# Optimization experiments

Hardware: AMD Instinct MI355X
Metric: run time of the kernel (lower is better)

## Reference

```python
import jax, jax.numpy as jnp
import numpy as np

B, S, D, H = 2, 2048, 2048, 16
HD = D // H          # head_dim = 128
FF = 8192            # intermediate_size
LN_EPS = 1e-05
BIT_EPS = 1e-05


def _rope_tables(seq_len, head_dim):
    inv_freq = 1.0 / (10000.0 ** (np.arange(0, head_dim, 2, dtype=np.float64) / head_dim))
    ang = np.arange(seq_len, dtype=np.float64)[:, None] * inv_freq[None, :]  # [S, HD/2]
    ang = np.concatenate([ang, ang], axis=-1)  # [S, HD]
    return jnp.asarray(np.cos(ang), jnp.float32), jnp.asarray(np.sin(ang), jnp.float32)


def setup_inputs() -> dict:
    key = jax.random.key(0)
    ks = jax.random.split(key, 9)
    hidden_states = jax.random.normal(ks[0], (B, S, D), jnp.float32)
    # causal additive mask [1, S, S]
    causal = jnp.tril(jnp.ones((S, S), bool))
    attention_mask = jnp.where(causal, 0.0, -1e9)[None].astype(jnp.float32)
    cos, sin = _rope_tables(S, HD)
    w = lambda k, o, i: jax.random.normal(k, (o, i), jnp.float32) * 0.02
    return {
        'hidden_states': hidden_states,
        'attention_mask': attention_mask,
        'cos': cos, 'sin': sin,
        'wq': w(ks[1], D, D), 'wk': w(ks[2], D, D),
        'wv': w(ks[3], D, D), 'wo': w(ks[4], D, D),
        'wg': w(ks[5], FF, D), 'wu': w(ks[6], FF, D), 'wd': w(ks[7], D, FF),
        'ln1_w': jnp.ones((D,), jnp.float32),
        'ln2_w': jnp.ones((D,), jnp.float32),
    }


def bitlinear(x, w):
    # ternarize: clamp(round(w / (mean|w| + eps)), -1, 1); int8 cast in torch
    # breaks grad through the ternary values -> stop_gradient here.
    scale = jnp.mean(jnp.abs(w))
    tern = jax.lax.stop_gradient(jnp.clip(jnp.round(w / (scale + BIT_EPS)), -1.0, 1.0))
    # dequant = ternary * mean|w|, then standard linear (x @ W^T)
    return jnp.einsum('bsi,oi->bso', x, tern * scale)


def rmsnorm(x, w, eps=LN_EPS):
    var = jnp.mean(jnp.square(x.astype(jnp.float32)), axis=-1, keepdims=True)
    return w * (x * jax.lax.rsqrt(var + eps))


def rotate_half(x):
    x1, x2 = jnp.split(x, 2, axis=-1)
    return jnp.concatenate([-x2, x1], axis=-1)


def apply_rope(q, k, cos, sin):
    # q, k: [B, S, D] -> per-head rope -> back to [B, S, D]
    qh = q.reshape(B, S, H, HD)
    kh = k.reshape(B, S, H, HD)
    c = cos[None, :, None, :]
    s = sin[None, :, None, :]
    qe = qh * c + rotate_half(qh) * s
    ke = kh * c + rotate_half(kh) * s
    return qe.reshape(B, S, D), ke.reshape(B, S, D)


def reference(hidden_states, attention_mask, cos, sin,
              wq, wk, wv, wo, wg, wu, wd, ln1_w, ln2_w):
    residual = hidden_states
    # --- attention block ---
    x = rmsnorm(hidden_states, ln1_w)
    q = bitlinear(x, wq)
    k = bitlinear(x, wk)
    v = bitlinear(x, wv)
    q, k = apply_rope(q, k, cos, sin)
    # NOTE: scores over FULL hidden dim (no head split), scaled by sqrt(head_dim),
    # exactly as in the original module.
    scores = jnp.einsum('bsd,btd->bst', q, k) / jnp.sqrt(jnp.float32(HD))
    scores = scores + attention_mask
    probs = jax.nn.softmax(scores, axis=-1)
    attn_out = jnp.einsum('bst,btd->bsd', probs, v)
    attn_out = bitlinear(attn_out, wo)
    h = residual + attn_out
    # --- MLP block ---
    residual = h
    y = rmsnorm(h, ln2_w)
    gated = bitlinear(y, wg) * bitlinear(y, wu)
    out = bitlinear(gated, wd)
    return residual + out
```

## Files before the change

### kernel.cpp

```cpp
#include <hip/hip_runtime.h>
#include <stdint.h>

#define DEV __device__ __forceinline__

typedef __attribute__((ext_vector_type(8))) short short8;
typedef __attribute__((ext_vector_type(8))) __bf16 bf16x8;
typedef __attribute__((ext_vector_type(4))) float f32x4;

DEV unsigned short f2bf(float f) {
  union { float f; unsigned int u; } v; v.f = f;
  unsigned int r = v.u + 0x7fffu + ((v.u >> 16) & 1u);
  return (unsigned short)(r >> 16);
}
DEV float bf2f(unsigned short h) {
  union { unsigned int u; float f; } v; v.u = ((unsigned int)h) << 16;
  return v.f;
}
DEV f32x4 mfma16(short8 a, short8 b, f32x4 c) {
  return __builtin_amdgcn_mfma_f32_16x16x32_bf16(
      __builtin_bit_cast(bf16x8, a), __builtin_bit_cast(bf16x8, b), c, 0, 0, 0);
}
DEV void gload_lds16(const void* g, void* lds) {
  __builtin_amdgcn_global_load_lds(
      (const __attribute__((address_space(1))) void*)g,
      (__attribute__((address_space(3))) void*)lds, 16, 0, 0);
}

struct MArgs {
  const float* src[7];
  unsigned short* dst[7];
  int n[7];
  int sidx[7];
};

__global__ __launch_bounds__(256) void absmean_partial_multi(
    MArgs a, float* __restrict__ partial) {
  const int m = blockIdx.y;
  const float4* w4 = (const float4*)a.src[m];
  const int n4 = a.n[m] >> 2;
  float s = 0.f;
  for (int i = blockIdx.x * 256 + threadIdx.x; i < n4; i += 1024 * 256) {
    float4 v = w4[i];
    s += fabsf(v.x) + fabsf(v.y) + fabsf(v.z) + fabsf(v.w);
  }
#pragma unroll
  for (int mm = 1; mm < 64; mm <<= 1) s += __shfl_xor(s, mm);
  __shared__ float red[4];
  if ((threadIdx.x & 63) == 0) red[threadIdx.x >> 6] = s;
  __syncthreads();
  if (threadIdx.x == 0)
    partial[m * 1024 + blockIdx.x] = red[0] + red[1] + red[2] + red[3];
}

__global__ __launch_bounds__(256) void absmean_final(
    const float* __restrict__ partial, float* __restrict__ scales) {
  __shared__ double red[256];
  const int m = blockIdx.x;
  double s = 0.0;
  for (int i = threadIdx.x; i < 1024; i += 256) s += (double)partial[m * 1024 + i];
  red[threadIdx.x] = s;
  __syncthreads();
  for (int t = 128; t > 0; t >>= 1) {
    if (threadIdx.x < t) red[threadIdx.x] += red[threadIdx.x + t];
    __syncthreads();
  }
  if (threadIdx.x == 0) {
    const long long cnt = (m < 4) ? 4194304ll : 16777216ll;
    scales[m] = (float)(red[0] / (double)cnt);
  }
}

__global__ __launch_bounds__(256) void quantize_multi(
    MArgs a, const float* __restrict__ scales) {
  const int m = blockIdx.y;
  const float sc = scales[a.sidx[m]];
  const float inv = 1.f / (sc + 1e-5f);
  const float4* src = (const float4*)a.src[m];
  ushort4* dst = (ushort4*)a.dst[m];
  const int n4 = a.n[m] >> 2;
  for (int i = blockIdx.x * 256 + threadIdx.x; i < n4; i += 2048 * 256) {
    float4 v = src[i];
    ushort4 o;
    o.x = f2bf(fminf(fmaxf(rintf(v.x * inv), -1.f), 1.f) * sc);
    o.y = f2bf(fminf(fmaxf(rintf(v.y * inv), -1.f), 1.f) * sc);
    o.z = f2bf(fminf(fmaxf(rintf(v.z * inv), -1.f), 1.f) * sc);
    o.w = f2bf(fminf(fmaxf(rintf(v.w * inv), -1.f), 1.f) * sc);
    dst[i] = o;
  }
}

__global__ __launch_bounds__(256) void rmsnorm_k(
    const float* __restrict__ x, const float* __restrict__ wt,
    unsigned short* __restrict__ out) {
  const long long t = blockIdx.x;
  const float* xr = x + t * 2048;
  const int i0 = threadIdx.x * 8;
  float4 a = *(const float4*)(xr + i0);
  float4 b = *(const float4*)(xr + i0 + 4);
  float ss = a.x * a.x + a.y * a.y + a.z * a.z + a.w * a.w +
             b.x * b.x + b.y * b.y + b.z * b.z + b.w * b.w;
#pragma unroll
  for (int m = 1; m < 64; m <<= 1) ss += __shfl_xor(ss, m);
  __shared__ float red[4];
  if ((threadIdx.x & 63) == 0) red[threadIdx.x >> 6] = ss;
  __syncthreads();
  float tot = red[0] + red[1] + red[2] + red[3];
  float rs = rsqrtf(tot * (1.f / 2048.f) + 1e-5f);
  float4 wa = *(const float4*)(wt + i0);
  float4 wb = *(const float4*)(wt + i0 + 4);
  ushort4 o1, o2;
  o1.x = f2bf(a.x * wa.x * rs); o1.y = f2bf(a.y * wa.y * rs);
  o1.z = f2bf(a.z * wa.z * rs); o1.w = f2bf(a.w * wa.w * rs);
  o2.x = f2bf(b.x * wb.x * rs); o2.y = f2bf(b.y * wb.y * rs);
  o2.z = f2bf(b.z * wb.z * rs); o2.w = f2bf(b.w * wb.w * rs);
  *(ushort4*)(out + t * 2048 + i0) = o1;
  *(ushort4*)(out + t * 2048 + i0 + 4) = o2;
}

__global__ __launch_bounds__(256) void combine_rms(
    const float* __restrict__ ep, const unsigned short* __restrict__ p,
    const float* __restrict__ wt, float* __restrict__ hout,
    unsigned short* __restrict__ yout) {
  const long long t = blockIdx.x;
  const int i0 = threadIdx.x * 8;
  const long long base = t * 2048 + i0;
  float4 e1 = *(const float4*)(ep + base);
  float4 e2 = *(const float4*)(ep + base + 4);
  short8 pa = *(const short8*)(p + base);
  short8 pb = *(const short8*)(p + 8388608 + base);
  const float e[8] = {e1.x, e1.y, e1.z, e1.w, e2.x, e2.y, e2.z, e2.w};
  float h[8];
#pragma unroll
  for (int i = 0; i < 8; ++i)
    h[i] = e[i] + bf2f((unsigned short)pa[i]) + bf2f((unsigned short)pb[i]);
  float4 h1 = {h[0], h[1], h[2], h[3]};
  float4 h2 = {h[4], h[5], h[6], h[7]};
  *(float4*)(hout + base) = h1;
  *(float4*)(hout + base + 4) = h2;
  float ss = 0.f;
#pragma unroll
  for (int i = 0; i < 8; ++i) ss += h[i] * h[i];
#pragma unroll
  for (int m = 1; m < 64; m <<= 1) ss += __shfl_xor(ss, m);
  __shared__ float red[4];
  if ((threadIdx.x & 63) == 0) red[threadIdx.x >> 6] = ss;
  __syncthreads();
  const float tot = red[0] + red[1] + red[2] + red[3];
  const float rs = rsqrtf(tot * (1.f / 2048.f) + 1e-5f);
  float4 wa = *(const float4*)(wt + i0);
  float4 wb = *(const float4*)(wt + i0 + 4);
  ushort4 o1, o2;
  o1.x = f2bf(h[0] * wa.x * rs); o1.y = f2bf(h[1] * wa.y * rs);
  o1.z = f2bf(h[2] * wa.z * rs); o1.w = f2bf(h[3] * wa.w * rs);
  o2.x = f2bf(h[4] * wb.x * rs); o2.y = f2bf(h[5] * wb.y * rs);
  o2.z = f2bf(h[6] * wb.z * rs); o2.w = f2bf(h[7] * wb.w * rs);
  *(ushort4*)(yout + base) = o1;
  *(ushort4*)(yout + base + 4) = o2;
}

__global__ __launch_bounds__(256) void combine2(
    const float* __restrict__ ep, const unsigned short* __restrict__ p,
    float* __restrict__ out) {
  const long long base = (long long)blockIdx.x * 2048 + threadIdx.x * 8;
  float4 e1 = *(const float4*)(ep + base);
  float4 e2 = *(const float4*)(ep + base + 4);
  short8 pa = *(const short8*)(p + base);
  short8 pb = *(const short8*)(p + 8388608 + base);
  float4 o1, o2;
  o1.x = e1.x + bf2f((unsigned short)pa[0]) + bf2f((unsigned short)pb[0]);
  o1.y = e1.y + bf2f((unsigned short)pa[1]) + bf2f((unsigned short)pb[1]);
  o1.z = e1.z + bf2f((unsigned short)pa[2]) + bf2f((unsigned short)pb[2]);
  o1.w = e1.w + bf2f((unsigned short)pa[3]) + bf2f((unsigned short)pb[3]);
  o2.x = e2.x + bf2f((unsigned short)pa[4]) + bf2f((unsigned short)pb[4]);
  o2.y = e2.y + bf2f((unsigned short)pa[5]) + bf2f((unsigned short)pb[5]);
  o2.z = e2.z + bf2f((unsigned short)pa[6]) + bf2f((unsigned short)pb[6]);
  o2.w = e2.w + bf2f((unsigned short)pa[7]) + bf2f((unsigned short)pb[7]);
  *(float4*)(out + base) = o1;
  *(float4*)(out + base + 4) = o2;
}

__global__ __launch_bounds__(256) void rope_k(
    const unsigned short* __restrict__ qkv, const float* __restrict__ cosT,
    const float* __restrict__ sinT, unsigned short* __restrict__ qr,
    unsigned short* __restrict__ kr) {
  const long long gid = (long long)blockIdx.x * 256 + threadIdx.x;
  const int t = (int)(gid >> 10);
  const int r = (int)(gid & 1023);
  const int h = r >> 6, d = r & 63;
  const int s = t & 2047;
  const unsigned short* row = qkv + (long long)t * 6144;
  const float c = cosT[s * 128 + d], sn = sinT[s * 128 + d];
  const int col = h * 128 + d;
  const float SC = 0.08838834764831845f;
  float q1 = bf2f(row[col]), q2 = bf2f(row[col + 64]);
  float k1 = bf2f(row[2048 + col]), k2 = bf2f(row[2048 + col + 64]);
  long long ob = (long long)t * 2048 + col;
  qr[ob] = f2bf((q1 * c - q2 * sn) * SC);
  qr[ob + 64] = f2bf((q2 * c + q1 * sn) * SC);
  kr[ob] = f2bf(k1 * c - k2 * sn);
  kr[ob + 64] = f2bf(k2 * c + k1 * sn);
}

__global__ __launch_bounds__(256) void vtrans_k(
    const unsigned short* __restrict__ qkv, unsigned short* __restrict__ vt) {
  __shared__ unsigned short tile[64][66];
  const int tt = blockIdx.x << 6, dd = blockIdx.y << 6;
  const long long b = blockIdx.z;
  const int r0 = threadIdx.x >> 4, c0 = (threadIdx.x & 15) << 2;
#pragma unroll
  for (int i = 0; i < 4; ++i) {
    const int row = r0 + i * 16;
    ushort4 v = *(const ushort4*)&qkv[(b * 2048 + tt + row) * 6144 + 4096 + dd + c0];
    tile[row][c0] = v.x; tile[row][c0 + 1] = v.y;
    tile[row][c0 + 2] = v.z; tile[row][c0 + 3] = v.w;
  }
  __syncthreads();
#pragma unroll
  for (int i = 0; i < 4; ++i) {
    const int d = r0 + i * 16;
    ushort4 o;
    o.x = tile[c0][d]; o.y = tile[c0 + 1][d];
    o.z = tile[c0 + 2][d]; o.w = tile[c0 + 3][d];
    *(ushort4*)&vt[(b * 2048 + dd + d) * 2048 + tt + c0] = o;
  }
}

__global__ __launch_bounds__(256) void softmax_causal(
    const float* __restrict__ scores, unsigned short* __restrict__ probs) {
  const int r = blockIdx.x;
  const int s = r & 2047;
  const float* src = scores + (long long)r * 2048;
  unsigned short* dst = probs + (long long)r * 2048;
  const int L = s + 1;
  const int j0 = threadIdx.x * 8;
  float4 a = *(const float4*)(src + j0);
  float4 b = *(const float4*)(src + j0 + 4);
  float v[8] = {a.x, a.y, a.z, a.w, b.x, b.y, b.z, b.w};
  float mx = -1e30f;
#pragma unroll
  for (int i = 0; i < 8; ++i) {
    if (j0 + i >= L) v[i] = -1e30f;
    mx = fmaxf(mx, v[i]);
  }
#pragma unroll
  for (int m = 1; m < 64; m <<= 1) mx = fmaxf(mx, __shfl_xor(mx, m));
  __shared__ float redM[4], redS[4];
  if ((threadIdx.x & 63) == 0) redM[threadIdx.x >> 6] = mx;
  __syncthreads();
  mx = fmaxf(fmaxf(redM[0], redM[1]), fmaxf(redM[2], redM[3]));
  float sum = 0.f;
#pragma unroll
  for (int i = 0; i < 8; ++i) {
    v[i] = (j0 + i < L) ? __expf(v[i] - mx) : 0.f;
    sum += v[i];
  }
#pragma unroll
  for (int m = 1; m < 64; m <<= 1) sum += __shfl_xor(sum, m);
  if ((threadIdx.x & 63) == 0) redS[threadIdx.x >> 6] = sum;
  __syncthreads();
  const float inv = 1.f / (redS[0] + redS[1] + redS[2] + redS[3]);
  ushort4 o1, o2;
  o1.x = f2bf(v[0] * inv); o1.y = f2bf(v[1] * inv);
  o1.z = f2bf(v[2] * inv); o1.w = f2bf(v[3] * inv);
  o2.x = f2bf(v[4] * inv); o2.y = f2bf(v[5] * inv);
  o2.z = f2bf(v[6] * inv); o2.w = f2bf(v[7] * inv);
  *(ushort4*)(dst + j0) = o1;
  *(ushort4*)(dst + j0 + 4) = o2;
}

template <int EPI, int CAUSAL>
__global__ __launch_bounds__(256) void gemm_nt(
    const unsigned short* __restrict__ A, const unsigned short* __restrict__ Bw,
    void* __restrict__ Cp, int M, int N, int K,
    long long sAz, long long sBz, long long sCz) {
  const long long m0 = (long long)blockIdx.y * 128;
  const long long n0 = (long long)blockIdx.x * 128;
  if (CAUSAL == 1 && n0 > m0 + 127) return;
  __shared__ __align__(16) unsigned short sA[2][128 * 32];
  __shared__ __align__(16) unsigned short sB[2][128 * 32];
  const int tid = threadIdx.x;
  const int w = tid >> 6, l = tid & 63;
  const long long z = blockIdx.z;
  A += z * sAz;
  Bw += z * sBz;
  const long long cofs = z * sCz;
  const int wr = w >> 1, wc = w & 1;
  const int lrow = l & 15, lk = (l >> 4) * 8;

  f32x4 acc[4][4] = {};
  int nk = K >> 5;
  if (CAUSAL == 2) nk = (int)((m0 + 128) >> 5);
  int cur = 0;

  auto stage = [&](int buf, int k0) {
#pragma unroll
    for (int i = 0; i < 2; ++i) {
      const int flat = (w * 2 + i) * 64 + l;
      const int row = flat >> 2;
      const int col = (flat & 3) * 8;
      gload_lds16(&A[(m0 + row) * K + k0 + col], (char*)&sA[buf][0] + (w * 2 + i) * 1024);
      gload_lds16(&Bw[(n0 + row) * K + k0 + col], (char*)&sB[buf][0] + (w * 2 + i) * 1024);
    }
  };

  stage(0, 0);
  __syncthreads();
  for (int kt = 0; kt < nk; ++kt) {
    if (kt + 1 < nk) stage(cur ^ 1, (kt + 1) << 5);
    short8 af[4], bfr[4];
#pragma unroll
    for (int m = 0; m < 4; ++m)
      af[m] = *(const short8*)&sA[cur][(wr * 64 + m * 16 + lrow) * 32 + lk];
#pragma unroll
    for (int n = 0; n < 4; ++n)
      bfr[n] = *(const short8*)&sB[cur][(wc * 64 + n * 16 + lrow) * 32 + lk];
#pragma unroll
    for (int m = 0; m < 4; ++m)
#pragma unroll
      for (int n = 0; n < 4; ++n)
        acc[m][n] = mfma16(af[m], bfr[n], acc[m][n]);
    __syncthreads();
    cur ^= 1;
  }

  const int orow = (l >> 4) * 4, ocol = l & 15;
#pragma unroll
  for (int m = 0; m < 4; ++m)
#pragma unroll
    for (int n = 0; n < 4; ++n)
#pragma unroll
      for (int r = 0; r < 4; ++r) {
        long long gr = m0 + wr * 64 + m * 16 + orow + r;
        long long gc = n0 + wc * 64 + n * 16 + ocol;
        long long idx = cofs + gr * N + gc;
        float v = acc[m][n][r];
        if (EPI == 0) ((unsigned short*)Cp)[idx] = f2bf(v);
        else ((float*)Cp)[idx] = v;
      }
}

template <int EPI, int CAUSAL>
__global__ __launch_bounds__(512, 2) void gemm256(
    const unsigned short* __restrict__ A, const unsigned short* __restrict__ Bw,
    void* __restrict__ Cp, const void* __restrict__ Ep,
    int N, int K, int nbx, int kLen, int ngTot,
    long long sAz, long long sBz, long long zCout) {
  __shared__ __align__(16) unsigned short lds[4 * 2 * 8192];
  __shared__ __align__(16) unsigned short ldsDummy[512];
  const int tid = threadIdx.x;
  const int wid = tid >> 6, l = tid & 63;
  const int wr = wid >> 2, wcn = wid & 3;

  const int nwg = gridDim.x;
  const int q8 = nwg >> 3;
  const int lin = (blockIdx.x & 7) * q8 + (blockIdx.x >> 3);
  const int t32 = lin >> 5, r32 = lin & 31;
  const int tpr = nbx >> 3;
  const int tm = t32 / tpr, tn = t32 - tm * tpr;
  const long long m0 = (long long)(tm * 4 + (r32 >> 3)) * 256;
  const long long n0 = (long long)(tn * 8 + (r32 & 7)) * 256;
  if (CAUSAL == 1 && n0 > m0) return;
  const int z = blockIdx.z;
  A += z * sAz;
  Bw += z * sBz;
  const long long kbase = (long long)z * kLen;
  const long long zofs = (long long)z * zCout;
  int ng = ngTot;
  if (CAUSAL == 2) {
    const int lim = (int)((m0 + 256) >> 5);
    ng = lim < ng ? lim : ng;
  }

  const int stRow = (l >> 2);
  const int stCol = (((l & 3) ^ ((l >> 3) & 3))) * 8;
  auto stage = [&](int chunk, int sslot) {
    if (chunk < ng) {
      char* base = (char*)lds + (sslot * 2) * 16384;
      const long long kcol = kbase + (long long)chunk * 32 + stCol;
#pragma unroll
      for (int i = 0; i < 2; ++i) {
        const int row = (wid * 2 + i) * 16 + stRow;
        gload_lds16(&A[(m0 + row) * K + kcol], base + (wid * 2 + i) * 1024);
        gload_lds16(&Bw[(n0 + row) * K + kcol],
                    base + 16384 + (wid * 2 + i) * 1024);
      }
    } else {
#pragma unroll
      for (int i = 0; i < 4; ++i) gload_lds16(&A[m0 * K], (char*)ldsDummy);
    }
  };

  const int ar = l & 15;
  const int rj = ((l >> 4) ^ ((l >> 1) & 3)) << 4;
  const int aoff = (wr * 128 + ar) * 64 + rj;
  const int boff = (wcn * 64 + ar) * 64 + rj;

  f32x4 acc[8][4] = {};
  short8 aX[4], bX[4], aY[4], bY[4];

  stage(0, 0); stage(1, 1); stage(2, 2);
  asm volatile("s_waitcnt vmcnt(4)" ::: "memory");
  __builtin_amdgcn_s_barrier();
#pragma unroll
  for (int m = 0; m < 4; ++m)
    aX[m] = *(const short8*)((const char*)lds + aoff + m * 1024);
#pragma unroll
  for (int n = 0; n < 4; ++n)
    bX[n] = *(const short8*)((const char*)lds + 16384 + boff + n * 1024);

#define CHUNK_BODY(SLOT, NSLOT, SYNC, cur03, curB, nxt03, nxtB, cc)            \
  {                                                                            \
    const char* sAc = (const char*)lds + (SLOT * 2) * 16384;                   \
    const char* sAn = (const char*)lds + (NSLOT * 2) * 16384;                  \
    const char* sBn = (const char*)lds + (NSLOT * 2 + 1) * 16384;              \
    short8 a47[4];                                                             \
    _Pragma("unroll") for (int m = 0; m < 4; ++m)                              \
        a47[m] = *(const short8*)(sAc + aoff + 4096 + m * 1024);               \
    stage((cc) + 3, (SLOT + 3) & 3);                                           \
    __builtin_amdgcn_s_setprio(1);                                             \
    _Pragma("unroll") for (int m = 0; m < 4; ++m)                              \
      _Pragma("unroll") for (int n = 0; n < 4; ++n)                            \
          acc[m][n] = mfma16(cur03[m], curB[n], acc[m][n]);                    \
    __builtin_amdgcn_s_setprio(0);                                             \
    if (SYNC) {                                                                \
      asm volatile("s_waitcnt vmcnt(4)" ::: "memory");                         \
      __builtin_amdgcn_s_barrier();                                            \
    }                                                                          \
    _Pragma("unroll") for (int m = 0; m < 4; ++m)                              \
        nxt03[m] = *(const short8*)(sAn + aoff + m * 1024);                    \
    _Pragma("unroll") for (int n = 0; n < 4; ++n)                              \
        nxtB[n] = *(const short8*)(sBn + boff + n * 1024);                     \
    __builtin_amdgcn_s_setprio(1);                                             \
    _Pragma("unroll") for (int m = 0; m < 4; ++m)                              \
      _Pragma("unroll") for (int n = 0; n < 4; ++n)                            \
          acc[m + 4][n] = mfma16(a47[m], curB[n], acc[m + 4][n]);              \
    __builtin_amdgcn_s_setprio(0);                                             \
  }

  for (int c = 0; c < ng; c += 4) {
    CHUNK_BODY(0, 1, false, aX, bX, aY, bY, c);
    CHUNK_BODY(1, 2, true, aY, bY, aX, bX, c + 1);
    CHUNK_BODY(2, 3, false, aX, bX, aY, bY, c + 2);
    CHUNK_BODY(3, 0, true, aY, bY, aX, bX, c + 3);
  }
#undef CHUNK_BODY
  asm volatile("s_waitcnt vmcnt(0)" ::: "memory");
  __builtin_amdgcn_s_barrier();

  const int orow = (l >> 4) * 4, ocol = l & 15;
#pragma unroll
  for (int m = 0; m < 8; ++m)
#pragma unroll
    for (int n = 0; n < 4; ++n)
#pragma unroll
      for (int r = 0; r < 4; ++r) {
        const long long gr = m0 + wr * 128 + m * 16 + orow + r;
        const long long gc = n0 + wcn * 64 + n * 16 + ocol;
        const long long idx = zofs + gr * N + gc;
        const float v = acc[m][n][r];
        if (EPI == 0) {
          ((unsigned short*)Cp)[idx] = f2bf(v);
        } else if (EPI == 2) {
          ((unsigned short*)Cp)[idx] = f2bf(bf2f(((const unsigned short*)Ep)[idx]) * v);
        } else {
          ((float*)Cp)[idx] = v;
        }
      }
}

extern "C" void kernel_launch(void* const* d_in, const int* in_sizes, int n_in,
                              void* d_out, int out_size, void* d_ws, size_t ws_size,
                              hipStream_t stream) {
  (void)in_sizes; (void)n_in; (void)out_size; (void)ws_size;
  const float* hidden = (const float*)d_in[0];
  const float* cosT = (const float*)d_in[2];
  const float* sinT = (const float*)d_in[3];
  const float* wq = (const float*)d_in[4];
  const float* wk = (const float*)d_in[5];
  const float* wv = (const float*)d_in[6];
  const float* wo = (const float*)d_in[7];
  const float* wg = (const float*)d_in[8];
  const float* wu = (const float*)d_in[9];
  const float* wd = (const float*)d_in[10];
  const float* ln1 = (const float*)d_in[11];
  const float* ln2 = (const float*)d_in[12];

  const size_t MB = 1ull << 20;
  char* ws = (char*)d_ws;
  unsigned short* xn    = (unsigned short*)(ws + 0);
  unsigned short* wqkvq = (unsigned short*)(ws + 16 * MB);
  unsigned short* qkv   = (unsigned short*)(ws + 40 * MB);
  unsigned short* qrb   = (unsigned short*)(ws + 88 * MB);
  unsigned short* krb   = (unsigned short*)(ws + 104 * MB);
  unsigned short* vtb   = (unsigned short*)(ws + 120 * MB);
  float*          scoresB = (float*)(ws + 0);
  unsigned short* probsB  = (unsigned short*)(ws + 40 * MB);
  unsigned short* partb = (unsigned short*)(ws + 0);
  unsigned short* wgq   = (unsigned short*)(ws + 0);
  unsigned short* wuq   = (unsigned short*)(ws + 32 * MB);
  unsigned short* gbuf  = (unsigned short*)(ws + 64 * MB);
  unsigned short* attnb = (unsigned short*)(ws + 136 * MB);
  unsigned short* woq   = (unsigned short*)(ws + 152 * MB);
  float*          hbuf  = (float*)(ws + 160 * MB);
  unsigned short* ybuf  = (unsigned short*)(ws + 192 * MB);
  unsigned short* gated = (unsigned short*)(ws + 208 * MB);
  unsigned short* wdq   = (unsigned short*)(ws + 272 * MB);
  float* wspart         = (float*)(ws + 304 * MB);
  float* scales         = (float*)(ws + 304 * MB + 32768);

  MArgs am;
  am.src[0] = wq; am.src[1] = wk; am.src[2] = wv; am.src[3] = wo;
  am.src[4] = wg; am.src[5] = wu; am.src[6] = wd;
  am.n[0] = am.n[1] = am.n[2] = am.n[3] = 4194304;
  am.n[4] = am.n[5] = am.n[6] = 16777216;
  for (int i = 0; i < 7; ++i) { am.dst[i] = nullptr; am.sidx[i] = i; }
  absmean_partial_multi<<<dim3(1024, 7), 256, 0, stream>>>(am, wspart);
  absmean_final<<<7, 256, 0, stream>>>(wspart, scales);

  MArgs qe;
  qe.src[0] = wq; qe.dst[0] = wqkvq;            qe.n[0] = 4194304;  qe.sidx[0] = 0;
  qe.src[1] = wk; qe.dst[1] = wqkvq + 4194304;  qe.n[1] = 4194304;  qe.sidx[1] = 1;
  qe.src[2] = wv; qe.dst[2] = wqkvq + 8388608;  qe.n[2] = 4194304;  qe.sidx[2] = 2;
  qe.src[3] = wo; qe.dst[3] = woq;              qe.n[3] = 4194304;  qe.sidx[3] = 3;
  qe.src[4] = wd; qe.dst[4] = wdq;              qe.n[4] = 16777216; qe.sidx[4] = 6;
  qe.src[5] = wq; qe.dst[5] = nullptr; qe.n[5] = 0; qe.sidx[5] = 0;
  qe.src[6] = wq; qe.dst[6] = nullptr; qe.n[6] = 0; qe.sidx[6] = 0;
  quantize_multi<<<dim3(2048, 5), 256, 0, stream>>>(qe, scales);

  rmsnorm_k<<<4096, 256, 0, stream>>>(hidden, ln1, xn);

  gemm256<0, 0><<<dim3(384, 1, 1), 512, 0, stream>>>(
      xn, wqkvq, qkv, nullptr, 6144, 2048, 24, 2048, 64, 0, 0, 0);

  rope_k<<<16384, 256, 0, stream>>>(qkv, cosT, sinT, qrb, krb);
  vtrans_k<<<dim3(32, 32, 2), 256, 0, stream>>>(qkv, vtb);

  gemm_nt<4, 1><<<dim3(16, 16, 2), 256, 0, stream>>>(
      qrb, krb, scoresB, 2048, 2048, 2048, 4194304, 4194304, 4194304);
  softmax_causal<<<4096, 256, 0, stream>>>(scoresB, probsB);
  gemm_nt<0, 2><<<dim3(16, 16, 2), 256, 0, stream>>>(
      probsB, vtb, attnb, 2048, 2048, 2048, 4194304, 4194304, 4194304);

  gemm256<0, 0><<<dim3(128, 1, 2), 512, 0, stream>>>(
      attnb, woq, partb, nullptr, 2048, 2048, 8, 1024, 32, 0, 0, 8388608);
  combine_rms<<<4096, 256, 0, stream>>>(hidden, partb, ln2, hbuf, ybuf);

  MArgs ql;
  ql.src[0] = wg; ql.dst[0] = wgq; ql.n[0] = 16777216; ql.sidx[0] = 4;
  ql.src[1] = wu; ql.dst[1] = wuq; ql.n[1] = 16777216; ql.sidx[1] = 5;
  for (int i = 2; i < 7; ++i) { ql.src[i] = wg; ql.dst[i] = nullptr; ql.n[i] = 0; ql.sidx[i] = 0; }
  quantize_multi<<<dim3(2048, 2), 256, 0, stream>>>(ql, scales);

  gemm256<0, 0><<<dim3(512, 1, 1), 512, 0, stream>>>(
      ybuf, wgq, gbuf, nullptr, 8192, 2048, 32, 2048, 64, 0, 0, 0);
  gemm256<2, 0><<<dim3(512, 1, 1), 512, 0, stream>>>(
      ybuf, wuq, gated, gbuf, 8192, 2048, 32, 2048, 64, 0, 0, 0);

  gemm256<0, 0><<<dim3(128, 1, 2), 512, 0, stream>>>(
      gated, wdq, partb, nullptr, 2048, 8192, 8, 4096, 128, 0, 0, 8388608);
  combine2<<<4096, 256, 0, stream>>>(hbuf, partb, (float*)d_out);
}
```

Baseline: 772.5 us.

## Restructure gemm256 to double-buffered 64-wide K tiles with phased barriers

Replaces the 4-slot, 32-wide K-chunk pipeline in gemm256 with a 2-buffer scheme using 64-wide K tiles split into two halves. Each tile runs four MFMA phases separated by barriers, with LDS waits and priority bumps, while the next tile's halves are prefetched. The unused CAUSAL template path is dropped. The intent is a more regular schedule with larger K steps and fewer stalls, at the cost of more barriers per tile and shallower prefetch depth.

```diff
diff --git a/kernel.cpp b/kernel.cpp
--- a/kernel.cpp
+++ b/kernel.cpp
@@ -339,14 +339,13 @@
       }
 }
 
-template <int EPI, int CAUSAL>
+template <int EPI>
 __global__ __launch_bounds__(512, 2) void gemm256(
     const unsigned short* __restrict__ A, const unsigned short* __restrict__ Bw,
     void* __restrict__ Cp, const void* __restrict__ Ep,
-    int N, int K, int nbx, int kLen, int ngTot,
+    int N, int K, int nbx, int kLen, int NT,
     long long sAz, long long sBz, long long zCout) {
-  __shared__ __align__(16) unsigned short lds[4 * 2 * 8192];
-  __shared__ __align__(16) unsigned short ldsDummy[512];
+  __shared__ __align__(16) unsigned short lds[2 * 2 * 2 * 8192];
   const int tid = threadIdx.x;
   const int wid = tid >> 6, l = tid & 63;
   const int wr = wid >> 2, wcn = wid & 3;
@@ -359,93 +358,104 @@
   const int tm = t32 / tpr, tn = t32 - tm * tpr;
   const long long m0 = (long long)(tm * 4 + (r32 >> 3)) * 256;
   const long long n0 = (long long)(tn * 8 + (r32 & 7)) * 256;
-  if (CAUSAL == 1 && n0 > m0) return;
   const int z = blockIdx.z;
   A += z * sAz;
   Bw += z * sBz;
   const long long kbase = (long long)z * kLen;
   const long long zofs = (long long)z * zCout;
-  int ng = ngTot;
-  if (CAUSAL == 2) {
-    const int lim = (int)((m0 + 256) >> 5);
-    ng = lim < ng ? lim : ng;
-  }
-
-  const int stRow = (l >> 2);
-  const int stCol = (((l & 3) ^ ((l >> 3) & 3))) * 8;
-  auto stage = [&](int chunk, int sslot) {
-    if (chunk < ng) {
-      char* base = (char*)lds + (sslot * 2) * 16384;
-      const long long kcol = kbase + (long long)chunk * 32 + stCol;
-#pragma unroll
-      for (int i = 0; i < 2; ++i) {
-        const int row = (wid * 2 + i) * 16 + stRow;
-        gload_lds16(&A[(m0 + row) * K + kcol], base + (wid * 2 + i) * 1024);
-        gload_lds16(&Bw[(n0 + row) * K + kcol],
-                    base + 16384 + (wid * 2 + i) * 1024);
-      }
-    } else {
-#pragma unroll
-      for (int i = 0; i < 4; ++i) gload_lds16(&A[m0 * K], (char*)ldsDummy);
+
+  const int sRow = tid >> 2;
+  const int sCol = ((tid & 3) ^ ((sRow >> 1) & 3)) * 8;
+  auto stageH = [&](int tile, int matofs, int khalf, int bufofs) {
+    if (tile < NT) {
+      const unsigned short* src = matofs ? Bw : A;
+      const long long rb = matofs ? n0 : m0;
+      const long long kc = kbase + (long long)tile * 64 + khalf * 32 + sCol;
+      char* dst = (char*)lds + bufofs + matofs + khalf * 16384 + wid * 1024;
+      gload_lds16(&src[(rb + sRow) * K + kc], dst);
+      gload_lds16(&src[(rb + sRow + 128) * K + kc], dst + 8192);
     }
   };
 
   const int ar = l & 15;
   const int rj = ((l >> 4) ^ ((l >> 1) & 3)) << 4;
-  const int aoff = (wr * 128 + ar) * 64 + rj;
-  const int boff = (wcn * 64 + ar) * 64 + rj;
 
   f32x4 acc[8][4] = {};
-  short8 aX[4], bX[4], aY[4], bY[4];
-
-  stage(0, 0); stage(1, 1); stage(2, 2);
-  asm volatile("s_waitcnt vmcnt(4)" ::: "memory");
-  __builtin_amdgcn_s_barrier();
-#pragma unroll
-  for (int m = 0; m < 4; ++m)
-    aX[m] = *(const short8*)((const char*)lds + aoff + m * 1024);
-#pragma unroll
-  for (int n = 0; n < 4; ++n)
-    bX[n] = *(const short8*)((const char*)lds + 16384 + boff + n * 1024);
-
-#define CHUNK_BODY(SLOT, NSLOT, SYNC, cur03, curB, nxt03, nxtB, cc)            \
-  {                                                                            \
-    const char* sAc = (const char*)lds + (SLOT * 2) * 16384;                   \
-    const char* sAn = (const char*)lds + (NSLOT * 2) * 16384;                  \
-    const char* sBn = (const char*)lds + (NSLOT * 2 + 1) * 16384;              \
-    short8 a47[4];                                                             \
-    _Pragma("unroll") for (int m = 0; m < 4; ++m)                              \
-        a47[m] = *(const short8*)(sAc + aoff + 4096 + m * 1024);               \
-    stage((cc) + 3, (SLOT + 3) & 3);                                           \
-    __builtin_amdgcn_s_setprio(1);                                             \
-    _Pragma("unroll") for (int m = 0; m < 4; ++m)                              \
-      _Pragma("unroll") for (int n = 0; n < 4; ++n)                            \
-          acc[m][n] = mfma16(cur03[m], curB[n], acc[m][n]);                    \
-    __builtin_amdgcn_s_setprio(0);                                             \
-    if (SYNC) {                                                                \
-      asm volatile("s_waitcnt vmcnt(4)" ::: "memory");                         \
-      __builtin_amdgcn_s_barrier();                                            \
-    }                                                                          \
-    _Pragma("unroll") for (int m = 0; m < 4; ++m)                              \
-        nxt03[m] = *(const short8*)(sAn + aoff + m * 1024);                    \
-    _Pragma("unroll") for (int n = 0; n < 4; ++n)                              \
-        nxtB[n] = *(const short8*)(sBn + boff + n * 1024);                     \
-    __builtin_amdgcn_s_setprio(1);                                             \
-    _Pragma("unroll") for (int m = 0; m < 4; ++m)                              \
-      _Pragma("unroll") for (int n = 0; n < 4; ++n)                            \
-          acc[m + 4][n] = mfma16(a47[m], curB[n], acc[m + 4][n]);              \
-    __builtin_amdgcn_s_setprio(0);                                             \
-  }
-
-  for (int c = 0; c < ng; c += 4) {
-    CHUNK_BODY(0, 1, false, aX, bX, aY, bY, c);
-    CHUNK_BODY(1, 2, true, aY, bY, aX, bX, c + 1);
-    CHUNK_BODY(2, 3, false, aX, bX, aY, bY, c + 2);
-    CHUNK_BODY(3, 0, true, aY, bY, aX, bX, c + 3);
-  }
-#undef CHUNK_BODY
+
+  stageH(0, 0, 0, 0); stageH(0, 32768, 0, 0);
+  stageH(0, 0, 1, 0); stageH(0, 32768, 1, 0);
   asm volatile("s_waitcnt vmcnt(0)" ::: "memory");
   __builtin_amdgcn_s_barrier();
+
+#define PHASE_SYNC()                                                           \
+  __builtin_amdgcn_s_barrier();                                                \
+  asm volatile("s_waitcnt lgkmcnt(0)" ::: "memory");                           \
+  __builtin_amdgcn_sched_barrier(0);                                           \
+  __builtin_amdgcn_s_setprio(1);
+
+#define PHASE_END()                                                            \
+  __builtin_amdgcn_s_setprio(0);                                               \
+  __builtin_amdgcn_s_barrier();
+
+#define TILE(BUF, tt)                                                          \
+  {                                                                            \
+    const char* A0 = (const char*)lds + BUF * 65536;                           \
+    const char* A1 = A0 + 16384;                                               \
+    const char* B0 = A0 + 32768;                                               \
+    const char* B1 = A0 + 49152;                                               \
+    const int NB = (BUF ^ 1) * 65536;                                          \
+    short8 av[4], bv[4];                                                       \
+                            \
+    _Pragma("unroll") for (int m = 0; m < 4; ++m)                              \
+        av[m] = *(const short8*)(A0 + (wr * 128 + m * 16 + ar) * 64 + rj);     \
+    _Pragma("unroll") for (int n = 0; n < 4; ++n)                              \
+        bv[n] = *(const short8*)(B0 + (wcn * 64 + n * 16 + ar) * 64 + rj);     \
+    stageH((tt) + 1, 0, 0, NB);                                                \
+    stageH((tt) + 1, 32768, 0, NB);                                            \
+    PHASE_SYNC();                                                              \
+    _Pragma("unroll") for (int m = 0; m < 4; ++m)                              \
+      _Pragma("unroll") for (int n = 0; n < 4; ++n)                            \
+          acc[m][n] = mfma16(av[m], bv[n], acc[m][n]);                         \
+    PHASE_END();                                                               \
+                 \
+    _Pragma("unroll") for (int m = 0; m < 4; ++m)                              \
+        av[m] = *(const short8*)(A0 + (wr * 128 + (m + 4) * 16 + ar) * 64 + rj); \
+    stageH((tt) + 1, 0, 1, NB);                                                \
+    stageH((tt) + 1, 32768, 1, NB);                                            \
+    PHASE_SYNC();                                                              \
+    _Pragma("unroll") for (int m = 0; m < 4; ++m)                              \
+      _Pragma("unroll") for (int n = 0; n < 4; ++n)                            \
+          acc[m + 4][n] = mfma16(av[m], bv[n], acc[m + 4][n]);                 \
+    PHASE_END();                                                               \
+                                                \
+    _Pragma("unroll") for (int m = 0; m < 4; ++m)                              \
+        av[m] = *(const short8*)(A1 + (wr * 128 + m * 16 + ar) * 64 + rj);     \
+    _Pragma("unroll") for (int n = 0; n < 4; ++n)                              \
+        bv[n] = *(const short8*)(B1 + (wcn * 64 + n * 16 + ar) * 64 + rj);     \
+    PHASE_SYNC();                                                              \
+    _Pragma("unroll") for (int m = 0; m < 4; ++m)                              \
+      _Pragma("unroll") for (int n = 0; n < 4; ++n)                            \
+          acc[m][n] = mfma16(av[m], bv[n], acc[m][n]);                         \
+    PHASE_END();                                                               \
+      \
+    _Pragma("unroll") for (int m = 0; m < 4; ++m)                              \
+        av[m] = *(const short8*)(A1 + (wr * 128 + (m + 4) * 16 + ar) * 64 + rj); \
+    PHASE_SYNC();                                                              \
+    _Pragma("unroll") for (int m = 0; m < 4; ++m)                              \
+      _Pragma("unroll") for (int n = 0; n < 4; ++n)                            \
+          acc[m + 4][n] = mfma16(av[m], bv[n], acc[m + 4][n]);                 \
+    __builtin_amdgcn_s_setprio(0);                                             \
+    asm volatile("s_waitcnt vmcnt(0)" ::: "memory");                           \
+    __builtin_amdgcn_s_barrier();                                              \
+  }
+
+  for (int t = 0; t < NT; t += 2) {
+    TILE(0, t);
+    TILE(1, t + 1);
+  }
+#undef TILE
+#undef PHASE_SYNC
+#undef PHASE_END
 
   const int orow = (l >> 4) * 4, ocol = l & 15;
 #pragma unroll
@@ -529,8 +539,8 @@
 
   rmsnorm_k<<<4096, 256, 0, stream>>>(hidden, ln1, xn);
 
-  gemm256<0, 0><<<dim3(384, 1, 1), 512, 0, stream>>>(
-      xn, wqkvq, qkv, nullptr, 6144, 2048, 24, 2048, 64, 0, 0, 0);
+  gemm256<0><<<dim3(384, 1, 1), 512, 0, stream>>>(
+      xn, wqkvq, qkv, nullptr, 6144, 2048, 24, 2048, 32, 0, 0, 0);
 
   rope_k<<<16384, 256, 0, stream>>>(qkv, cosT, sinT, qrb, krb);
   vtrans_k<<<dim3(32, 32, 2), 256, 0, stream>>>(qkv, vtb);
@@ -541,8 +551,8 @@
   gemm_nt<0, 2><<<dim3(16, 16, 2), 256, 0, stream>>>(
       probsB, vtb, attnb, 2048, 2048, 2048, 4194304, 4194304, 4194304);
 
-  gemm256<0, 0><<<dim3(128, 1, 2), 512, 0, stream>>>(
-      attnb, woq, partb, nullptr, 2048, 2048, 8, 1024, 32, 0, 0, 8388608);
+  gemm256<0><<<dim3(128, 1, 2), 512, 0, stream>>>(
+      attnb, woq, partb, nullptr, 2048, 2048, 8, 1024, 16, 0, 0, 8388608);
   combine_rms<<<4096, 256, 0, stream>>>(hidden, partb, ln2, hbuf, ybuf);
 
   MArgs ql;
@@ -551,12 +561,12 @@
   for (int i = 2; i < 7; ++i) { ql.src[i] = wg; ql.dst[i] = nullptr; ql.n[i] = 0; ql.sidx[i] = 0; }
   quantize_multi<<<dim3(2048, 2), 256, 0, stream>>>(ql, scales);
 
-  gemm256<0, 0><<<dim3(512, 1, 1), 512, 0, stream>>>(
-      ybuf, wgq, gbuf, nullptr, 8192, 2048, 32, 2048, 64, 0, 0, 0);
-  gemm256<2, 0><<<dim3(512, 1, 1), 512, 0, stream>>>(
-      ybuf, wuq, gated, gbuf, 8192, 2048, 32, 2048, 64, 0, 0, 0);
-
-  gemm256<0, 0><<<dim3(128, 1, 2), 512, 0, stream>>>(
-      gated, wdq, partb, nullptr, 2048, 8192, 8, 4096, 128, 0, 0, 8388608);
+  gemm256<0><<<dim3(512, 1, 1), 512, 0, stream>>>(
+      ybuf, wgq, gbuf, nullptr, 8192, 2048, 32, 2048, 32, 0, 0, 0);
+  gemm256<2><<<dim3(512, 1, 1), 512, 0, stream>>>(
+      ybuf, wuq, gated, gbuf, 8192, 2048, 32, 2048, 32, 0, 0, 0);
+
+  gemm256<0><<<dim3(128, 1, 2), 512, 0, stream>>>(
+      gated, wdq, partb, nullptr, 2048, 8192, 8, 4096, 64, 0, 0, 8388608);
   combine2<<<4096, 256, 0, stream>>>(hbuf, partb, (float*)d_out);
 }
```

After: 871.6 us. +12.8%, slower.
